# Performance work log

Measured on AMD Instinct MI355X. Metric: run time of the kernel, lower is better.

Reference implementation:

```python
import jax, jax.numpy as jnp
import numpy as np

B, S, D, H, L, F = 1, 2048, 768, 12, 2, 3072
DH = D // H          # 64
W = 256              # one-sided sliding window (attention_window=512 total)
NC = S // W          # number of query chunks
VOCAB = 50265


def _ln(x, s, b, eps=1e-5):
    m = x.mean(-1, keepdims=True)
    v = ((x - m) ** 2).mean(-1, keepdims=True)
    return (x - m) / jnp.sqrt(v + eps) * s + b


def setup_inputs() -> dict:
    key = jax.random.key(0)
    ks = jax.random.split(key, 16)
    p = lambda k, sh: jax.random.normal(k, sh, jnp.float32) * 0.02
    return {
        "input_ids": jax.random.randint(ks[0], (B, S), 0, VOCAB),
        "attention_mask": jnp.ones((B, S), jnp.int32),
        "word_emb": p(ks[1], (VOCAB, D)),
        "pos_emb": p(ks[2], (S + 2, D)),          # roberta-style pos ids start at 2
        "type_emb": p(ks[3], (1, D)),
        "emb_ln_s": jnp.ones((D,), jnp.float32),
        "emb_ln_b": jnp.zeros((D,), jnp.float32),
        "Wqkv": p(ks[4], (L, 3, D, D)),
        "bqkv": jnp.zeros((L, 3, D), jnp.float32),
        "Wo": p(ks[5], (L, D, D)),
        "bo": jnp.zeros((L, D), jnp.float32),
        "ln1_s": jnp.ones((L, D), jnp.float32),
        "ln1_b": jnp.zeros((L, D), jnp.float32),
        "W1": p(ks[6], (L, D, F)),
        "b1": jnp.zeros((L, F), jnp.float32),
        "W2": p(ks[7], (L, F, D)),
        "b2": jnp.zeros((L, D), jnp.float32),
        "ln2_s": jnp.ones((L, D), jnp.float32),
        "ln2_b": jnp.zeros((L, D), jnp.float32),
        "pool_W": p(ks[8], (D, D)),
        "pool_b": jnp.zeros((D,), jnp.float32),
    }


def reference(input_ids, attention_mask, word_emb, pos_emb, type_emb,
              emb_ln_s, emb_ln_b, Wqkv, bqkv, Wo, bo, ln1_s, ln1_b,
              W1, b1, W2, b2, ln2_s, ln2_b, pool_W, pool_b):
    # ---- embeddings (roberta/longformer style) ----
    pos_ids = jnp.cumsum(attention_mask, axis=1) * attention_mask + 1  # padding_idx=1
    x = word_emb[input_ids] + pos_emb[pos_ids] + type_emb[0]
    x = _ln(x, emb_ln_s, emb_ln_b)

    # ---- banded-attention index/mask precompute (int constants) ----
    idx = jnp.arange(NC)[:, None] * W + jnp.arange(3 * W)[None, :]      # [NC, 3W] into padded seq
    rel = (jnp.arange(3 * W)[None, :] - W) - jnp.arange(W)[:, None]     # key_pos - query_pos
    band = (rel >= -W) & (rel <= W)                                      # [W, 3W]
    kmask = jnp.pad(attention_mask, ((0, 0), (W, W)))[:, idx].astype(bool)  # [B, NC, 3W]
    valid = band[None, None] & kmask[:, :, None, :]                      # [B, NC, W, 3W]

    inv_sqrt_dh = 1.0 / np.sqrt(DH)
    for l in range(L):
        qkv = jnp.einsum('bsd,tde->tbse', x, Wqkv[l]) + bqkv[l][:, None, None, :]
        q, k, v = [t.reshape(B, S, H, DH).transpose(0, 2, 1, 3) for t in qkv]  # [B,H,S,DH]
        qc = q.reshape(B, H, NC, W, DH)
        kp = jnp.pad(k, ((0, 0), (0, 0), (W, W), (0, 0)))
        vp = jnp.pad(v, ((0, 0), (0, 0), (W, W), (0, 0)))
        kc = kp[:, :, idx]                                               # [B,H,NC,3W,DH]
        vc = vp[:, :, idx]
        scores = jnp.einsum('bhcqd,bhckd->bhcqk', qc, kc) * inv_sqrt_dh  # [B,H,NC,W,3W]
        scores = jnp.where(valid[:, None], scores, -1e9)
        attn = jax.nn.softmax(scores, axis=-1)
        ctx = jnp.einsum('bhcqk,bhckd->bhcqd', attn, vc)
        ctx = ctx.reshape(B, H, S, DH).transpose(0, 2, 1, 3).reshape(B, S, D)
        x = _ln(x + ctx @ Wo[l] + bo[l], ln1_s[l], ln1_b[l])
        h = jax.nn.gelu(x @ W1[l] + b1[l], approximate=False)
        x = _ln(x + h @ W2[l] + b2[l], ln2_s[l], ln2_b[l])

    pooled = jnp.tanh(x[:, 0] @ pool_W + pool_b)
    return x, pooled
```

## Files before the change

### kernel.cpp

```cpp
#include <hip/hip_runtime.h>
#include <hip/hip_bf16.h>
#include <math.h>
#include <stddef.h>
#include <stdint.h>

typedef __hip_bfloat16 bf16;
typedef short bf16x8 __attribute__((ext_vector_type(8)));
typedef float f32x4 __attribute__((ext_vector_type(4)));

#define CS 2048
#define CD 768
#define CH 12
#define CDH 64
#define CF 3072
#define CW 256
#define CL 2
#define QKVN 2304
#define SDC ((size_t)CS * CD)

__device__ __forceinline__ void gload_lds16(const bf16* g, bf16* l) {
  __builtin_amdgcn_global_load_lds(
      (const __attribute__((address_space(1))) void*)g,
      (__attribute__((address_space(3))) void*)l, 16, 0, 0);
}

__device__ __forceinline__ unsigned short f2bu(float v) {
  bf16 b = __float2bfloat16(v);
  return *(unsigned short*)&b;
}

__device__ __forceinline__ float block_reduce_sum(float v, float* buf) {
  #pragma unroll
  for (int off = 32; off > 0; off >>= 1) v += __shfl_down(v, off, 64);
  int wid = threadIdx.x >> 6;
  __syncthreads();
  if ((threadIdx.x & 63) == 0) buf[wid] = v;
  __syncthreads();
  if (threadIdx.x == 0) buf[0] = buf[0] + buf[1] + buf[2] + buf[3];
  __syncthreads();
  return buf[0];
}

__global__ __launch_bounds__(256) void scan_kernel(const int* __restrict__ mask,
                                                   int* __restrict__ pos) {
  __shared__ int part[256];
  int tid = threadIdx.x;
  int mv[8]; int s = 0;
  #pragma unroll
  for (int i = 0; i < 8; ++i) { mv[i] = mask[tid * 8 + i]; s += mv[i]; }
  part[tid] = s;
  __syncthreads();
  for (int off = 1; off < 256; off <<= 1) {
    int t = 0;
    if (tid >= off) t = part[tid - off];
    __syncthreads();
    part[tid] += t;
    __syncthreads();
  }
  int run = part[tid] - s;
  #pragma unroll
  for (int i = 0; i < 8; ++i) {
    run += mv[i];
    pos[tid * 8 + i] = run * mv[i] + 1;
  }
}

__global__ __launch_bounds__(256) void transpose_all(
    const float* __restrict__ Wqkv, const float* __restrict__ Wo,
    const float* __restrict__ W1, const float* __restrict__ W2,
    bf16* __restrict__ WqkvT, bf16* __restrict__ WoT,
    bf16* __restrict__ W1T, bf16* __restrict__ W2T) {
  __shared__ float tile[32][33];
  int b = blockIdx.x;
  const float* src; bf16* dst; int K, N, t;
  if (b < 3456) {
    int mat = b / 576; t = b % 576; K = 768; N = 768;
    src = Wqkv + (size_t)mat * 768 * 768; dst = WqkvT + (size_t)mat * 768 * 768;
  } else if (b < 4608) {
    b -= 3456; int mat = b / 576; t = b % 576; K = 768; N = 768;
    src = Wo + (size_t)mat * 768 * 768; dst = WoT + (size_t)mat * 768 * 768;
  } else if (b < 9216) {
    b -= 4608; int mat = b / 2304; t = b % 2304; K = 768; N = 3072;
    src = W1 + (size_t)mat * 768 * 3072; dst = W1T + (size_t)mat * 768 * 3072;
  } else {
    b -= 9216; int mat = b / 2304; t = b % 2304; K = 3072; N = 768;
    src = W2 + (size_t)mat * 3072 * 768; dst = W2T + (size_t)mat * 3072 * 768;
  }
  int nt = N / 32;
  int bn = (t % nt) * 32, bk = (t / nt) * 32;
  int tx = threadIdx.x & 31, ty = (threadIdx.x >> 5) & 7;
  #pragma unroll
  for (int i = 0; i < 32; i += 8)
    tile[ty + i][tx] = src[(size_t)(bk + ty + i) * N + bn + tx];
  __syncthreads();
  #pragma unroll
  for (int i = 0; i < 32; i += 8)
    dst[(size_t)(bn + ty + i) * K + bk + tx] = __float2bfloat16(tile[tx][ty + i]);
}

__global__ __launch_bounds__(256) void embed_ln_kernel(
    const int* __restrict__ ids, const int* __restrict__ pos,
    const float* __restrict__ wemb, const float* __restrict__ pemb,
    const float* __restrict__ temb, const float* __restrict__ gs,
    const float* __restrict__ gb, float* __restrict__ x, bf16* __restrict__ xb) {
  __shared__ float red[4];
  int srow = blockIdx.x;
  long long id = ids[srow];
  long long pid = pos[srow];
  float v[3];
  #pragma unroll
  for (int i = 0; i < 3; ++i) {
    int d = threadIdx.x + i * 256;
    v[i] = wemb[id * CD + d] + pemb[pid * CD + d] + temb[d];
  }
  float sum = v[0] + v[1] + v[2];
  sum = block_reduce_sum(sum, red);
  float mean = sum * (1.0f / CD);
  float sq = 0.f;
  #pragma unroll
  for (int i = 0; i < 3; ++i) { float c = v[i] - mean; sq += c * c; }
  sq = block_reduce_sum(sq, red);
  float rstd = rsqrtf(sq * (1.0f / CD) + 1e-5f);
  #pragma unroll
  for (int i = 0; i < 3; ++i) {
    int d = threadIdx.x + i * 256;
    float o = (v[i] - mean) * rstd * gs[d] + gb[d];
    x[(size_t)srow * CD + d] = o;
    xb[(size_t)srow * CD + d] = __float2bfloat16(o);
  }
}

template<int GELU, int OUTBF16, int SPLITS, int VTFUSE>
__global__ __launch_bounds__(256) void gemm_mfma(
    const bf16* __restrict__ A, const bf16* __restrict__ Bt,
    const float* __restrict__ bias, void* __restrict__ Cout,
    bf16* __restrict__ vTout, int M, int N, int Ktot) {
  __shared__ __align__(16) bf16 As[128 * 32];
  __shared__ __align__(16) bf16 Bs[128 * 32];
  const int tid = threadIdx.x;
  const int wave = tid >> 6, lane = tid & 63;
  const int m0 = blockIdx.y * 128, n0 = blockIdx.x * 128;
  const int wm = (wave & 1) * 64, wn = (wave >> 1) * 64;
  const int quad = lane >> 4, rsel = lane & 15;
  const int r_in = lane >> 2;
  const int chunk = lane & 3;
  const int Klen = Ktot / SPLITS;
  const int koff = (SPLITS > 1) ? blockIdx.z * Klen : 0;

  f32x4 acc[4][4] = {};

  for (int k0 = 0; k0 < Klen; k0 += 32) {
    #pragma unroll
    for (int i = 0; i < 4; ++i) {
      int op = wave * 4 + i;
      if (op < 8) {
        int row = op * 16 + r_in;
        gload_lds16(A + (size_t)(m0 + row) * Ktot + koff + k0 + chunk * 8, &As[op * 512]);
      } else {
        int row = (op - 8) * 16 + r_in;
        gload_lds16(Bt + (size_t)(n0 + row) * Ktot + koff + k0 + chunk * 8, &Bs[(op - 8) * 512]);
      }
    }
    __syncthreads();
    bf16x8 af[4], bfr[4];
    #pragma unroll
    for (int i = 0; i < 4; ++i)
      af[i] = *(const bf16x8*)&As[(wm + i * 16 + rsel) * 32 + quad * 8];
    #pragma unroll
    for (int j = 0; j < 4; ++j)
      bfr[j] = *(const bf16x8*)&Bs[(wn + j * 16 + rsel) * 32 + quad * 8];
    #pragma unroll
    for (int i = 0; i < 4; ++i)
      #pragma unroll
      for (int j = 0; j < 4; ++j)
        acc[i][j] = __builtin_amdgcn_mfma_f32_16x16x32_bf16(af[i], bfr[j], acc[i][j], 0, 0, 0);
    __syncthreads();
  }
  #pragma unroll
  for (int j = 0; j < 4; ++j) {
    int col = n0 + wn + j * 16 + rsel;
    float bv = (SPLITS == 1 || blockIdx.z == 0) ? bias[col] : 0.f;
    if (VTFUSE && col >= 1536) {
      #pragma unroll
      for (int i = 0; i < 4; ++i) {
        int rowb = m0 + wm + i * 16 + quad * 4;
        ushort4 pk;
        pk.x = f2bu(acc[i][j][0] + bv);
        pk.y = f2bu(acc[i][j][1] + bv);
        pk.z = f2bu(acc[i][j][2] + bv);
        pk.w = f2bu(acc[i][j][3] + bv);
        *(ushort4*)&vTout[(size_t)(col - 1536) * CS + rowb] = pk;
      }
    } else {
      #pragma unroll
      for (int i = 0; i < 4; ++i) {
        #pragma unroll
        for (int r = 0; r < 4; ++r) {
          int rowm = m0 + wm + i * 16 + quad * 4 + r;
          float v = acc[i][j][r] + bv;
          if (GELU) v = 0.5f * v * (1.0f + erff(v * 0.70710678118654752f));
          if (OUTBF16) ((bf16*)Cout)[(size_t)rowm * N + col] = __float2bfloat16(v);
          else ((float*)Cout)[(size_t)blockIdx.z * M * N + (size_t)rowm * N + col] = v;
        }
      }
    }
  }
}

__global__ __launch_bounds__(512) void attn_mfma(
    const bf16* __restrict__ qkv, const bf16* __restrict__ vT,
    const int* __restrict__ mask, bf16* __restrict__ ctx) {
  __shared__ bf16 Ps[8][16][72];
  __shared__ float Obuf[4][16][64];
  __shared__ float Mbuf[4][16];
  __shared__ float Lbuf[4][16];
  const int h = blockIdx.y;
  const int q0 = blockIdx.x * 64;
  const int tid = threadIdx.x;
  const int wv = tid >> 6, lane = tid & 63;
  const int qg = wv & 3, half = wv >> 2;
  const int quad = lane >> 4, rsel = lane & 15;
  const int qw = q0 + qg * 16;

  const bf16* qp = &qkv[(size_t)(qw + rsel) * QKVN + h * CDH + quad * 8];
  bf16x8 qf0 = *(const bf16x8*)qp;
  bf16x8 qf1 = *(const bf16x8*)(qp + 32);

  float mi[4], li[4];
  f32x4 o[4] = {};
  #pragma unroll
  for (int r = 0; r < 4; ++r) { mi[r] = -1e30f; li[r] = 0.f; }

  const int kt0 = half ? 5 : 0, kt1 = half ? 9 : 5;
  #pragma unroll 1
  for (int kt = kt0; kt < kt1; ++kt) {
    int kbase = qw - CW + kt * 64;
    if (kbase + 63 < 0 || kbase >= CS) continue;

    f32x4 sc[4];
    #pragma unroll
    for (int nt = 0; nt < 4; ++nt) {
      int pp = kbase + nt * 16 + rsel;
      int ppc = min(max(pp, 0), CS - 1);
      const bf16* kp = &qkv[(size_t)ppc * QKVN + 768 + h * CDH + quad * 8];
      bf16x8 kf0 = *(const bf16x8*)kp;
      bf16x8 kf1 = *(const bf16x8*)(kp + 32);
      f32x4 z = {};
      z = __builtin_amdgcn_mfma_f32_16x16x32_bf16(qf0, kf0, z, 0, 0, 0);
      z = __builtin_amdgcn_mfma_f32_16x16x32_bf16(qf1, kf1, z, 0, 0, 0);
      sc[nt] = z;
    }
    float mx[4] = {-1e30f, -1e30f, -1e30f, -1e30f};
    #pragma unroll
    for (int nt = 0; nt < 4; ++nt) {
      int pp = kbase + nt * 16 + rsel;
      int ppc = min(max(pp, 0), CS - 1);
      bool kvld = (pp >= 0) && (pp < CS) && (mask[ppc] != 0);
      #pragma unroll
      for (int r = 0; r < 4; ++r) {
        int qr = qw + quad * 4 + r;
        float s = sc[nt][r] * 0.125f;
        bool band = (pp >= qr - CW) && (pp <= qr + CW);
        s = (kvld && band) ? s : -1e9f;
        sc[nt][r] = s;
        mx[r] = fmaxf(mx[r], s);
      }
    }
    #pragma unroll
    for (int r = 0; r < 4; ++r) {
      #pragma unroll
      for (int off = 1; off < 16; off <<= 1)
        mx[r] = fmaxf(mx[r], __shfl_xor(mx[r], off, 64));
    }
    float al[4], rs[4] = {};
    #pragma unroll
    for (int r = 0; r < 4; ++r) {
      float mn = fmaxf(mi[r], mx[r]);
      al[r] = __expf(mi[r] - mn);
      mi[r] = mn;
    }
    #pragma unroll
    for (int nt = 0; nt < 4; ++nt)
      #pragma unroll
      for (int r = 0; r < 4; ++r) {
        float p = __expf(sc[nt][r] - mi[r]);
        sc[nt][r] = p;
        rs[r] += p;
      }
    #pragma unroll
    for (int r = 0; r < 4; ++r) {
      #pragma unroll
      for (int off = 1; off < 16; off <<= 1)
        rs[r] += __shfl_xor(rs[r], off, 64);
      li[r] = li[r] * al[r] + rs[r];
    }
    #pragma unroll
    for (int d = 0; d < 4; ++d)
      #pragma unroll
      for (int r = 0; r < 4; ++r) o[d][r] *= al[r];
    #pragma unroll
    for (int nt = 0; nt < 4; ++nt)
      #pragma unroll
      for (int r = 0; r < 4; ++r)
        Ps[wv][quad * 4 + r][nt * 16 + rsel] = __float2bfloat16(sc[nt][r]);
    __asm__ volatile("s_waitcnt lgkmcnt(0)" ::: "memory");
    bf16x8 pf0 = *(const bf16x8*)&Ps[wv][rsel][quad * 8];
    bf16x8 pf1 = *(const bf16x8*)&Ps[wv][rsel][32 + quad * 8];
    int kc0 = min(max(kbase + quad * 8, 0), CS - 8);
    int kc1 = min(max(kbase + 32 + quad * 8, 0), CS - 8);
    #pragma unroll
    for (int d = 0; d < 4; ++d) {
      const bf16* vrow = &vT[(size_t)(h * CDH + d * 16 + rsel) * CS];
      bf16x8 vf0 = *(const bf16x8*)(vrow + kc0);
      bf16x8 vf1 = *(const bf16x8*)(vrow + kc1);
      o[d] = __builtin_amdgcn_mfma_f32_16x16x32_bf16(pf0, vf0, o[d], 0, 0, 0);
      o[d] = __builtin_amdgcn_mfma_f32_16x16x32_bf16(pf1, vf1, o[d], 0, 0, 0);
    }
  }

  if (half == 1) {
    #pragma unroll
    for (int d = 0; d < 4; ++d)
      #pragma unroll
      for (int r = 0; r < 4; ++r)
        Obuf[qg][quad * 4 + r][d * 16 + rsel] = o[d][r];
    if (rsel == 0) {
      #pragma unroll
      for (int r = 0; r < 4; ++r) {
        Mbuf[qg][quad * 4 + r] = mi[r];
        Lbuf[qg][quad * 4 + r] = li[r];
      }
    }
  }
  __syncthreads();
  if (half == 0) {
    #pragma unroll
    for (int r = 0; r < 4; ++r) {
      int row = quad * 4 + r;
      float m1 = Mbuf[qg][row], l1 = Lbuf[qg][row];
      float mn = fmaxf(mi[r], m1);
      float a0 = __expf(mi[r] - mn);
      float a1 = __expf(m1 - mn);
      float inv = 1.0f / (li[r] * a0 + l1 * a1);
      #pragma unroll
      for (int d = 0; d < 4; ++d) {
        float val = (o[d][r] * a0 + Obuf[qg][row][d * 16 + rsel] * a1) * inv;
        ctx[(size_t)(qw + row) * CD + h * CDH + d * 16 + rsel] = __float2bfloat16(val);
      }
    }
  }
}

template<int P>
__global__ __launch_bounds__(256) void add_ln_kernel(
    const float* __restrict__ g, const float* __restrict__ xin,
    float* __restrict__ xout, bf16* __restrict__ xb,
    const float* __restrict__ gs, const float* __restrict__ gb) {
  __shared__ float red[4];
  int srow = blockIdx.x;
  float v[3];
  #pragma unroll
  for (int i = 0; i < 3; ++i) {
    int d = threadIdx.x + i * 256;
    size_t idx = (size_t)srow * CD + d;
    float a = xin[idx];
    #pragma unroll
    for (int p = 0; p < P; ++p) a += g[p * SDC + idx];
    v[i] = a;
  }
  float sum = v[0] + v[1] + v[2];
  sum = block_reduce_sum(sum, red);
  float mean = sum * (1.0f / CD);
  float sq = 0.f;
  #pragma unroll
  for (int i = 0; i < 3; ++i) { float c = v[i] - mean; sq += c * c; }
  sq = block_reduce_sum(sq, red);
  float rstd = rsqrtf(sq * (1.0f / CD) + 1e-5f);
  #pragma unroll
  for (int i = 0; i < 3; ++i) {
    int d = threadIdx.x + i * 256;
    float o = (v[i] - mean) * rstd * gs[d] + gb[d];
    xout[(size_t)srow * CD + d] = o;
    xb[(size_t)srow * CD + d] = __float2bfloat16(o);
  }
}

__global__ __launch_bounds__(256) void pool_kernel(
    const float* __restrict__ x, const float* __restrict__ Wp,
    const float* __restrict__ bp, float* __restrict__ out) {
  __shared__ float xs[CD];
  __shared__ float red[4][64];
  int t = threadIdx.x;
  for (int i = t; i < CD; i += 256) xs[i] = x[i];
  __syncthreads();
  int n = blockIdx.x * 64 + (t & 63);
  int kp = t >> 6;
  float acc = 0.f;
  #pragma unroll 4
  for (int kk = kp * 192; kk < kp * 192 + 192; ++kk)
    acc = fmaf(xs[kk], Wp[(size_t)kk * CD + n], acc);
  red[kp][t & 63] = acc;
  __syncthreads();
  if (t < 64) {
    int nn = blockIdx.x * 64 + t;
    out[nn] = tanhf(red[0][t] + red[1][t] + red[2][t] + red[3][t] + bp[nn]);
  }
}

extern "C" void kernel_launch(void* const* d_in, const int* in_sizes, int n_in,
                              void* d_out, int out_size, void* d_ws, size_t ws_size,
                              hipStream_t stream) {
  const int*   ids   = (const int*)d_in[0];
  const int*   mask  = (const int*)d_in[1];
  const float* wemb  = (const float*)d_in[2];
  const float* pemb  = (const float*)d_in[3];
  const float* temb  = (const float*)d_in[4];
  const float* elns  = (const float*)d_in[5];
  const float* elnb  = (const float*)d_in[6];
  const float* Wqkv  = (const float*)d_in[7];
  const float* bqkv  = (const float*)d_in[8];
  const float* Wo    = (const float*)d_in[9];
  const float* bo    = (const float*)d_in[10];
  const float* ln1s  = (const float*)d_in[11];
  const float* ln1b  = (const float*)d_in[12];
  const float* W1    = (const float*)d_in[13];
  const float* b1    = (const float*)d_in[14];
  const float* W2    = (const float*)d_in[15];
  const float* b2    = (const float*)d_in[16];
  const float* ln2s  = (const float*)d_in[17];
  const float* ln2b  = (const float*)d_in[18];
  const float* poolW = (const float*)d_in[19];
  const float* poolb = (const float*)d_in[20];

  const size_t SD = SDC;
  const size_t SF = (size_t)CS * CF;

  char* w = (char*)d_ws;
  float* x    = (float*)w; w += SD * 4;
  bf16*  xb   = (bf16*)w;  w += SD * 2;
  bf16*  qkv  = (bf16*)w;  w += (size_t)CS * QKVN * 2;
  bf16*  vT   = (bf16*)w;  w += SD * 2;
  bf16*  ctxb = (bf16*)w;  w += SD * 2;
  bf16*  t1b  = (bf16*)w;  w += SF * 2;
  float* t2   = (float*)w; w += SD * 4 * 4;
  int*   pos  = (int*)w;   w += (size_t)CS * 4;
  bf16* WqkvT = (bf16*)w;  w += (size_t)CL * QKVN * CD * 2;
  bf16* WoT   = (bf16*)w;  w += (size_t)CL * CD * CD * 2;
  bf16* W1T   = (bf16*)w;  w += (size_t)CL * CF * CD * 2;
  bf16* W2T   = (bf16*)w;  w += (size_t)CL * CD * CF * 2;

  scan_kernel<<<1, 256, 0, stream>>>(mask, pos);
  transpose_all<<<13824, 256, 0, stream>>>(Wqkv, Wo, W1, W2, WqkvT, WoT, W1T, W2T);
  embed_ln_kernel<<<CS, 256, 0, stream>>>(ids, pos, wemb, pemb, temb, elns, elnb, x, xb);

  for (int l = 0; l < CL; ++l) {
    gemm_mfma<0,1,1,1><<<dim3(QKVN/128, CS/128), 256, 0, stream>>>(
        xb, WqkvT + (size_t)l * QKVN * CD, bqkv + (size_t)l * 3 * CD, qkv, vT, CS, QKVN, CD);
    attn_mfma<<<dim3(CS/64, CH), 512, 0, stream>>>(qkv, vT, mask, ctxb);
    gemm_mfma<0,0,2,0><<<dim3(CD/128, CS/128, 2), 256, 0, stream>>>(
        ctxb, WoT + (size_t)l * CD * CD, bo + (size_t)l * CD, t2, nullptr, CS, CD, CD);
    add_ln_kernel<2><<<CS, 256, 0, stream>>>(t2, x, x, xb,
        ln1s + (size_t)l * CD, ln1b + (size_t)l * CD);
    gemm_mfma<1,1,1,0><<<dim3(CF/128, CS/128), 256, 0, stream>>>(
        xb, W1T + (size_t)l * CF * CD, b1 + (size_t)l * CF, t1b, nullptr, CS, CF, CD);
    gemm_mfma<0,0,4,0><<<dim3(CD/128, CS/128, 4), 256, 0, stream>>>(
        t1b, W2T + (size_t)l * CD * CF, b2 + (size_t)l * CD, t2, nullptr, CS, CD, CF);
    float* lastx = (l == CL - 1) ? (float*)d_out : x;
    add_ln_kernel<4><<<CS, 256, 0, stream>>>(t2, x, lastx, xb,
        ln2s + (size_t)l * CD, ln2b + (size_t)l * CD);
  }

  pool_kernel<<<12, 256, 0, stream>>>((float*)d_out, poolW, poolb, (float*)d_out + SD);
}
```

Before: 598.7 us.

## Deepen GEMM K-tile with swizzled LDS, bf16 split-K partials, fuse position scan

The GEMM K-step grows from 32 to 64 and an XOR swizzle is applied to LDS chunk placement, which halves the barriers per K and is meant to cut bank conflicts. Split-K partial outputs are now stored as bf16 instead of fp32, halving traffic between the GEMM and the add+LayerNorm kernel at some cost in precision. The separate scan kernel is removed: each embedding block recomputes its prefix sum of the mask with a block reduction. That saves a launch but adds redundant O(S) reads per row.

```diff
diff --git a/kernel.cpp b/kernel.cpp
--- a/kernel.cpp
+++ b/kernel.cpp
@@ -39,30 +39,6 @@
   if (threadIdx.x == 0) buf[0] = buf[0] + buf[1] + buf[2] + buf[3];
   __syncthreads();
   return buf[0];
-}
-
-__global__ __launch_bounds__(256) void scan_kernel(const int* __restrict__ mask,
-                                                   int* __restrict__ pos) {
-  __shared__ int part[256];
-  int tid = threadIdx.x;
-  int mv[8]; int s = 0;
-  #pragma unroll
-  for (int i = 0; i < 8; ++i) { mv[i] = mask[tid * 8 + i]; s += mv[i]; }
-  part[tid] = s;
-  __syncthreads();
-  for (int off = 1; off < 256; off <<= 1) {
-    int t = 0;
-    if (tid >= off) t = part[tid - off];
-    __syncthreads();
-    part[tid] += t;
-    __syncthreads();
-  }
-  int run = part[tid] - s;
-  #pragma unroll
-  for (int i = 0; i < 8; ++i) {
-    run += mv[i];
-    pos[tid * 8 + i] = run * mv[i] + 1;
-  }
 }
 
 __global__ __launch_bounds__(256) void transpose_all(
@@ -99,14 +75,17 @@
 }
 
 __global__ __launch_bounds__(256) void embed_ln_kernel(
-    const int* __restrict__ ids, const int* __restrict__ pos,
+    const int* __restrict__ ids, const int* __restrict__ mask,
     const float* __restrict__ wemb, const float* __restrict__ pemb,
     const float* __restrict__ temb, const float* __restrict__ gs,
     const float* __restrict__ gb, float* __restrict__ x, bf16* __restrict__ xb) {
   __shared__ float red[4];
   int srow = blockIdx.x;
+  float ps = 0.f;
+  for (int i = threadIdx.x; i <= srow; i += 256) ps += (float)mask[i];
+  float tot = block_reduce_sum(ps, red);
+  long long pid = (long long)((int)(tot + 0.5f) * mask[srow] + 1);
   long long id = ids[srow];
-  long long pid = pos[srow];
   float v[3];
   #pragma unroll
   for (int i = 0; i < 3; ++i) {
@@ -135,45 +114,51 @@
     const bf16* __restrict__ A, const bf16* __restrict__ Bt,
     const float* __restrict__ bias, void* __restrict__ Cout,
     bf16* __restrict__ vTout, int M, int N, int Ktot) {
-  __shared__ __align__(16) bf16 As[128 * 32];
-  __shared__ __align__(16) bf16 Bs[128 * 32];
+  __shared__ __align__(16) bf16 As[128 * 64];
+  __shared__ __align__(16) bf16 Bs[128 * 64];
   const int tid = threadIdx.x;
   const int wave = tid >> 6, lane = tid & 63;
   const int m0 = blockIdx.y * 128, n0 = blockIdx.x * 128;
   const int wm = (wave & 1) * 64, wn = (wave >> 1) * 64;
   const int quad = lane >> 4, rsel = lane & 15;
-  const int r_in = lane >> 2;
-  const int chunk = lane & 3;
+  const int rx = rsel & 7;
+  const int r_in = lane >> 3;
+  const int chunk = lane & 7;
+  const int gchunk = chunk ^ r_in;
   const int Klen = Ktot / SPLITS;
   const int koff = (SPLITS > 1) ? blockIdx.z * Klen : 0;
 
   f32x4 acc[4][4] = {};
 
-  for (int k0 = 0; k0 < Klen; k0 += 32) {
-    #pragma unroll
-    for (int i = 0; i < 4; ++i) {
-      int op = wave * 4 + i;
-      if (op < 8) {
-        int row = op * 16 + r_in;
-        gload_lds16(A + (size_t)(m0 + row) * Ktot + koff + k0 + chunk * 8, &As[op * 512]);
+  for (int k0 = 0; k0 < Klen; k0 += 64) {
+    #pragma unroll
+    for (int i = 0; i < 8; ++i) {
+      int op = wave * 8 + i;
+      if (op < 16) {
+        int row = op * 8 + r_in;
+        gload_lds16(A + (size_t)(m0 + row) * Ktot + koff + k0 + gchunk * 8, &As[op * 512]);
       } else {
-        int row = (op - 8) * 16 + r_in;
-        gload_lds16(Bt + (size_t)(n0 + row) * Ktot + koff + k0 + chunk * 8, &Bs[(op - 8) * 512]);
+        int row = (op - 16) * 8 + r_in;
+        gload_lds16(Bt + (size_t)(n0 + row) * Ktot + koff + k0 + gchunk * 8, &Bs[(op - 16) * 512]);
       }
     }
     __syncthreads();
-    bf16x8 af[4], bfr[4];
-    #pragma unroll
-    for (int i = 0; i < 4; ++i)
-      af[i] = *(const bf16x8*)&As[(wm + i * 16 + rsel) * 32 + quad * 8];
-    #pragma unroll
-    for (int j = 0; j < 4; ++j)
-      bfr[j] = *(const bf16x8*)&Bs[(wn + j * 16 + rsel) * 32 + quad * 8];
-    #pragma unroll
-    for (int i = 0; i < 4; ++i)
+    #pragma unroll
+    for (int kh = 0; kh < 2; ++kh) {
+      bf16x8 af[4], bfr[4];
+      int cq = ((kh << 2) | quad);
+      #pragma unroll
+      for (int i = 0; i < 4; ++i)
+        af[i] = *(const bf16x8*)&As[(wm + i * 16 + rsel) * 64 + (cq ^ rx) * 8];
       #pragma unroll
       for (int j = 0; j < 4; ++j)
-        acc[i][j] = __builtin_amdgcn_mfma_f32_16x16x32_bf16(af[i], bfr[j], acc[i][j], 0, 0, 0);
+        bfr[j] = *(const bf16x8*)&Bs[(wn + j * 16 + rsel) * 64 + (cq ^ rx) * 8];
+      #pragma unroll
+      for (int i = 0; i < 4; ++i)
+        #pragma unroll
+        for (int j = 0; j < 4; ++j)
+          acc[i][j] = __builtin_amdgcn_mfma_f32_16x16x32_bf16(af[i], bfr[j], acc[i][j], 0, 0, 0);
+    }
     __syncthreads();
   }
   #pragma unroll
@@ -199,8 +184,12 @@
           int rowm = m0 + wm + i * 16 + quad * 4 + r;
           float v = acc[i][j][r] + bv;
           if (GELU) v = 0.5f * v * (1.0f + erff(v * 0.70710678118654752f));
-          if (OUTBF16) ((bf16*)Cout)[(size_t)rowm * N + col] = __float2bfloat16(v);
-          else ((float*)Cout)[(size_t)blockIdx.z * M * N + (size_t)rowm * N + col] = v;
+          if (SPLITS > 1)
+            ((bf16*)Cout)[(size_t)blockIdx.z * M * N + (size_t)rowm * N + col] = __float2bfloat16(v);
+          else if (OUTBF16)
+            ((bf16*)Cout)[(size_t)rowm * N + col] = __float2bfloat16(v);
+          else
+            ((float*)Cout)[(size_t)rowm * N + col] = v;
         }
       }
     }
@@ -353,7 +342,7 @@
 
 template<int P>
 __global__ __launch_bounds__(256) void add_ln_kernel(
-    const float* __restrict__ g, const float* __restrict__ xin,
+    const bf16* __restrict__ g, const float* __restrict__ xin,
     float* __restrict__ xout, bf16* __restrict__ xb,
     const float* __restrict__ gs, const float* __restrict__ gb) {
   __shared__ float red[4];
@@ -365,7 +354,7 @@
     size_t idx = (size_t)srow * CD + d;
     float a = xin[idx];
     #pragma unroll
-    for (int p = 0; p < P; ++p) a += g[p * SDC + idx];
+    for (int p = 0; p < P; ++p) a += __bfloat162float(g[p * SDC + idx]);
     v[i] = a;
   }
   float sum = v[0] + v[1] + v[2];
@@ -442,16 +431,14 @@
   bf16*  vT   = (bf16*)w;  w += SD * 2;
   bf16*  ctxb = (bf16*)w;  w += SD * 2;
   bf16*  t1b  = (bf16*)w;  w += SF * 2;
-  float* t2   = (float*)w; w += SD * 4 * 4;
-  int*   pos  = (int*)w;   w += (size_t)CS * 4;
+  bf16*  t2   = (bf16*)w;  w += SD * 2 * 4;
   bf16* WqkvT = (bf16*)w;  w += (size_t)CL * QKVN * CD * 2;
   bf16* WoT   = (bf16*)w;  w += (size_t)CL * CD * CD * 2;
   bf16* W1T   = (bf16*)w;  w += (size_t)CL * CF * CD * 2;
   bf16* W2T   = (bf16*)w;  w += (size_t)CL * CD * CF * 2;
 
-  scan_kernel<<<1, 256, 0, stream>>>(mask, pos);
   transpose_all<<<13824, 256, 0, stream>>>(Wqkv, Wo, W1, W2, WqkvT, WoT, W1T, W2T);
-  embed_ln_kernel<<<CS, 256, 0, stream>>>(ids, pos, wemb, pemb, temb, elns, elnb, x, xb);
+  embed_ln_kernel<<<CS, 256, 0, stream>>>(ids, mask, wemb, pemb, temb, elns, elnb, x, xb);
 
   for (int l = 0; l < CL; ++l) {
     gemm_mfma<0,1,1,1><<<dim3(QKVN/128, CS/128), 256, 0, stream>>>(
```

Result: faster. 561.2 us (-6.3%).
